# Kernel optimization log

Measured on AMD Instinct MI355X. Metric: run time of the kernel, lower is better.

The kernel has to match this reference:

```python
import jax, jax.numpy as jnp
import numpy as np
from jax import lax

# Module hyperparameters (init_kwargs)
B, T, F, H = 512, 256, 64, 128
D = F + H            # decoder LSTMCell width = input_dim + hidden_rnn
OUT_DIM = 32         # output_dim (survival horizon steps)
RISKS = 2
NEG = -1e10


def lstm_cell(x, h, c, Wih, Whh):
    # PyTorch gate order: i, f, g, o; bias=False
    g = x @ Wih.T + h @ Whh.T
    i, f, gg, o = jnp.split(g, 4, axis=-1)
    c = jax.nn.sigmoid(f) * c + jax.nn.sigmoid(i) * jnp.tanh(gg)
    h = jax.nn.sigmoid(o) * jnp.tanh(c)
    return h, c


def setup_inputs() -> dict:
    key = jax.random.key(0)
    ks = jax.random.split(key, 12)
    rn = lambda k, shp, fan: jax.random.normal(k, shp, jnp.float32) * (1.0 / np.sqrt(fan))
    return {
        "x": jax.random.normal(ks[0], (B, T, F), jnp.float32),
        # encoder LSTM (1 layer, bias=False)
        "W_ih_emb": rn(ks[1], (4 * H, F), F),
        "W_hh_emb": rn(ks[2], (4 * H, H), H),
        # longitudinal head: Linear(H -> F)
        "W_long": rn(ks[3], (F, H), H),
        "b_long": jnp.zeros((F,), jnp.float32),
        # attention head: Linear(F+H -> 1)
        "W_att": rn(ks[4], (1, D), D),
        "b_att": jnp.zeros((1,), jnp.float32),
        # per-risk cause-specific LSTMCell (bias=False) and Linear(D -> 1)
        "W_ih_cs": rn(ks[5], (RISKS, 4 * D, D), D),
        "W_hh_cs": rn(ks[6], (RISKS, 4 * D, D), D),
        "W_cs": rn(ks[7], (RISKS, 1, D), D),
        "b_cs": jnp.zeros((RISKS, 1), jnp.float32),
    }


def _forward(x, W_ih_emb, W_hh_emb, W_long, b_long, W_att, b_att,
             W_ih_cs, W_hh_cs, W_cs, b_cs):
    inputmask = jnp.abs(x).sum(2) == 0                      # [B,T]
    last_obs = (~inputmask).sum(axis=1) - 1                 # [B]

    # encoder LSTM over time
    def enc_step(carry, xt):
        h, c = carry
        h, c = lstm_cell(xt, h, c, W_ih_emb, W_hh_emb)
        return (h, c), h

    h0 = jnp.zeros((x.shape[0], H), x.dtype)
    _, hs = lax.scan(enc_step, (h0, h0), x.transpose(1, 0, 2))
    hidden = hs.transpose(1, 0, 2)                          # [B,T,H]

    long_pred = hidden @ W_long.T + b_long                  # [B,T,F]

    x_last = x[jnp.arange(x.shape[0]), last_obs]            # [B,F]
    concat = jnp.concatenate(
        [hidden, jnp.broadcast_to(x_last[:, None, :], (x.shape[0], x.shape[1], F))], -1)
    scores = (concat @ W_att.T + b_att)[..., 0]             # [B,T]

    idx = jnp.arange(x.shape[1])[None, :]
    scores = jnp.where(idx >= last_obs[:, None], NEG, scores)
    att = jax.nn.softmax(scores, axis=1)
    att = jnp.where((last_obs > 0)[:, None], att, 0.0)      # rows with last_obs==0 zeroed

    hidden_att = jnp.einsum('bt,bth->bh', att, hidden)      # [B,H]
    ha = jnp.concatenate([hidden_att, x_last], 1)           # [B,D]

    state0 = (lax.stop_gradient(ha), lax.stop_gradient(ha))  # .detach() on init state
    rs = jnp.arange(OUT_DIM * RISKS) % RISKS                # k-major, r-minor loop order

    def dec_step(carry, r):
        h, c = carry
        h, c = lstm_cell(ha, h, c, W_ih_cs[r], W_hh_cs[r])
        out = jax.nn.sigmoid(h @ W_cs[r].T + b_cs[r])       # [B,1]
        return (h, c), out

    _, outs = lax.scan(dec_step, state0, rs)                # [steps,B,1]
    outcomes = jax.nn.softmax(outs[..., 0].T, axis=-1)      # [B, OUT_DIM*RISKS]
    parts = tuple(outcomes[:, i * OUT_DIM:(i + 1) * OUT_DIM] for i in range(RISKS))
    return (long_pred,) + parts


def reference(x, W_ih_emb, W_hh_emb, W_long, b_long, W_att, b_att,
              W_ih_cs, W_hh_cs, W_cs, b_cs):
    return _forward(x, W_ih_emb, W_hh_emb, W_long, b_long, W_att, b_att,
                    W_ih_cs, W_hh_cs, W_cs, b_cs)
```

## Files before the change

### kernel.cpp

```cpp
#include <hip/hip_runtime.h>
#include <stdint.h>

#define DEV __device__ __forceinline__
typedef unsigned short u16; typedef unsigned int u32; typedef unsigned long long u64;
typedef __attribute__((ext_vector_type(8))) short s8v;
typedef __attribute__((ext_vector_type(4))) float f4v;

#define Bb 512
#define Tt 256
#define Ff 64
#define Hh 128
#define Dd 192
#define L2E  1.4426950408889634f
#define L2E2 2.8853900817779268f

DEV u16 f2bf(float f){ u32 u = __builtin_bit_cast(u32, f); u32 r = (u + 0x7fffu + ((u>>16)&1u)) >> 16; return (u16)r; }
DEV float sigm(float x){ return __builtin_amdgcn_rcpf(1.0f + __expf(-x)); }
DEV float ex2(float x){ float r; asm("v_exp_f32 %0, %1" : "=v"(r) : "v"(x)); return r; }
DEV float sig2n(float y){ return __builtin_amdgcn_rcpf(1.0f + ex2(y)); }
DEV float th2 (float y){ return 1.0f - 2.0f*__builtin_amdgcn_rcpf(1.0f + ex2(y)); }
DEV u32 cvtpk(float lo, float hi){ u32 d; asm("v_cvt_pk_bf16_f32 %0, %1, %2" : "=v"(d) : "v"(lo), "v"(hi)); return d; }
DEV float blo(u32 q){ return __builtin_bit_cast(float, q<<16); }
DEV float bhi(u32 q){ return __builtin_bit_cast(float, q & 0xffff0000u); }

DEV f4v mfma16(s8v a, s8v b, f4v c){ return __builtin_amdgcn_mfma_f32_16x16x32_bf16(a, b, c, 0, 0, 0); }
DEV void barrier_lds(){ asm volatile("s_waitcnt lgkmcnt(0)\n\ts_barrier" ::: "memory"); }

DEV void dma16(const void* g, void* l){
  __builtin_amdgcn_global_load_lds((const __attribute__((address_space(1))) void*)g,
                                   (__attribute__((address_space(3))) void*)l, 16, 0, 0);
}

DEV int hxe2(int k, int c){ return (k>>5)*512 + (((k>>3)&3)*16 + c)*8 + (k&7); }

DEV s8v pack8s(const float* p, float sc){
  const float4 a = *(const float4*)p; const float4 b = *(const float4*)(p+4);
  s8v r; r[0]=(short)f2bf(a.x*sc); r[1]=(short)f2bf(a.y*sc); r[2]=(short)f2bf(a.z*sc); r[3]=(short)f2bf(a.w*sc);
  r[4]=(short)f2bf(b.x*sc); r[5]=(short)f2bf(b.y*sc); r[6]=(short)f2bf(b.z*sc); r[7]=(short)f2bf(b.w*sc); return r;
}
DEV s8v pack8(const float* p){ return pack8s(p, 1.0f); }
DEV u32 pk2(float a, float b){ return (u32)f2bf(a) | ((u32)f2bf(b)<<16); }

__global__ __launch_bounds__(64) void prelim_k(const float* __restrict__ x,
    const float* __restrict__ Watt, const float* __restrict__ batt,
    float* __restrict__ xlast, float* __restrict__ c0, int* __restrict__ lastobs)
{
  int b = blockIdx.x, tid = threadIdx.x;
  int cnt = 0;
  for (int it = 0; it < 4; ++it){
    int t = it*64 + tid;
    const float4* p = (const float4*)(x + ((size_t)b*Tt + t)*Ff);
    float s = 0.0f;
    #pragma unroll
    for (int q = 0; q < 16; ++q){ float4 v = p[q]; s += fabsf(v.x)+fabsf(v.y)+fabsf(v.z)+fabsf(v.w); }
    u64 m = __ballot(s != 0.0f);
    cnt += __popcll(m);
  }
  int last = cnt - 1;
  int li = (last < 0) ? (Tt-1) : last;
  float xl = x[((size_t)b*Tt + li)*Ff + tid];
  xlast[b*Ff + tid] = xl;
  float p = xl * Watt[Hh + tid];
  for (int off = 32; off; off >>= 1) p += __shfl_down(p, off);
  if (tid == 0){ c0[b] = (p + batt[0]) * L2E; lastobs[b] = last; }
}

__global__ __launch_bounds__(256) void prep_wd_k(const float* __restrict__ Whhcs,
    const float* __restrict__ Wihcs, u16* __restrict__ Wd, u16* __restrict__ WdIH)
{
  int idx = blockIdx.x*256 + threadIdx.x;
  int j = idx & 7, lane = (idx>>3)&63;
  int f = idx>>9;
  int kt = f % 6; int mtr = f/6;
  int mt = mtr % 48, r = mtr/48;
  int ut = mt>>2, g = mt&3;
  int row = g*Dd + ut*16 + (lane&15);
  int k = kt*32 + (lane>>4)*8 + j;
  float sc = (g == 2) ? L2E2 : -L2E;
  size_t src = ((size_t)r*768 + row)*Dd + k;
  Wd[idx]   = f2bf(Whhcs[src] * sc);
  WdIH[idx] = f2bf(Wihcs[src] * sc);
}

__global__ __launch_bounds__(64) void xw_k(const u16* __restrict__ WdIH,
    const float* __restrict__ ha, u16* __restrict__ xwg)
{
  int lane = threadIdx.x, l15 = lane&15, l4 = lane>>4;
  int cg = blockIdx.x & 3, rm = blockIdx.x >> 2;
  s8v af[6];
  #pragma unroll
  for (int kt=0;kt<6;++kt) af[kt] = *(const s8v*)(WdIH + (size_t)(rm*6+kt)*512 + lane*8);
  #pragma unroll
  for (int ct=0; ct<8; ++ct){
    int c = cg*128 + ct*16 + l15;
    f4v a = {0,0,0,0};
    #pragma unroll
    for (int kt=0;kt<6;++kt){
      s8v b = pack8(ha + (size_t)c*Dd + kt*32 + l4*8);
      a = mfma16(af[kt], b, a);
    }
    int bg = cg*8 + ct;
    int base = bg*24576 + rm*256 + l15*16 + l4*4;
    *(u32*)&xwg[base]   = pk2(a[0], a[1]);
    *(u32*)&xwg[base+2] = pk2(a[2], a[3]);
  }
}

__global__ __launch_bounds__(512)
__attribute__((amdgpu_waves_per_eu(2,2)))
void enc_k(
    const float* __restrict__ x, const float* __restrict__ Whh, const float* __restrict__ Wih,
    const float* __restrict__ Wlong, const float* __restrict__ blong, const float* __restrict__ Watt,
    const float* __restrict__ xlast, const float* __restrict__ c0v, const int* __restrict__ lastobs,
    float* __restrict__ lp_out, float* __restrict__ ha)
{
  __shared__ __align__(16) u16 hx[2][3072];
  __shared__ float sarr[2][16];
  const int tid = threadIdx.x, wid = tid>>6, lane = tid&63, l15 = lane&15, l4 = lane>>4;
  const int b0 = blockIdx.x*16;
  const int xrow = tid>>5, xc2 = (tid&31)*2;

  s8v wf[4][6];
  #pragma unroll
  for (int mt = 0; mt < 4; ++mt){
    int gate = mt*Hh + wid*16 + l15;
    float sc = (mt == 2) ? L2E2 : -L2E;
    #pragma unroll
    for (int kt = 0; kt < 6; ++kt){
      int k0 = kt*32 + l4*8;
      if (kt < 4) wf[mt][kt] = pack8s(Whh + (size_t)gate*Hh + k0, sc);
      else        wf[mt][kt] = pack8s(Wih + (size_t)gate*Ff + (k0 - Hh), sc);
    }
  }
  s8v wfx[6];
  {
    s8v z = {0,0,0,0,0,0,0,0};
    #pragma unroll
    for (int kt = 0; kt < 6; ++kt) wfx[kt] = z;
    if (wid < 4){
      int f = wid*16 + l15;
      #pragma unroll
      for (int kt = 0; kt < 4; ++kt) wfx[kt] = pack8(Wlong + (size_t)f*Hh + kt*32 + l4*8);
    } else if (wid == 4 && l15 == 0){
      #pragma unroll
      for (int kt = 0; kt < 4; ++kt) wfx[kt] = pack8s(Watt + kt*32 + l4*8, L2E);
    }
  }
  float bl[4] = {0,0,0,0};
  if (wid < 4){
    #pragma unroll
    for (int j = 0; j < 4; ++j) bl[j] = blong[wid*16 + l4*4 + j];
  }
  const int   lastb = lastobs[b0 + l15];
  const float c0b   = c0v[b0 + l15];

  const int he0 = hxe2(wid*16 + l4*4, l15);
  const int xe0 = hxe2(Hh + xc2, xrow);
  float* lpb = lp_out + ((size_t)(b0+l15)*Tt)*Ff + wid*16 + l4*4;

  ((u64*)hx[0])[tid] = 0ull;
  {
    float2 xv = *(const float2*)(x + ((size_t)(b0+xrow)*Tt + 0)*Ff + xc2);
    *(u32*)&hx[0][xe0] = cvtpk(xv.x, xv.y);
  }
  float2 xa = *(const float2*)(x + ((size_t)(b0+xrow)*Tt + 1)*Ff + xc2);
  float2 xb;
  __syncthreads();

  float cst[4] = {0,0,0,0}, hp[4] = {0,0,0,0}, hpp[4] = {0,0,0,0};
  float accA[4] = {0,0,0,0}, mrun = -3.0e38f, zrun = 0.0f;

#define ENC_STEP(T_, CURB_, NXTB_, XC_, XN_) { \
    const int t = (T_); \
    s8v bf[6]; \
    _Pragma("unroll") \
    for (int kt = 0; kt < 6; ++kt) \
      bf[kt] = *(const s8v*)&hx[CURB_][kt*512 + lane*8]; \
    { int tp = t + 2; if (tp > Tt-1) tp = Tt-1; \
      XN_ = *(const float2*)(x + ((size_t)(b0+xrow)*Tt + tp)*Ff + xc2); } \
    f4v acc0 = {0,0,0,0}, acc1 = {0,0,0,0}, acc2 = {0,0,0,0}, acc3 = {0,0,0,0}, accx = {0,0,0,0}; \
    _Pragma("unroll") \
    for (int kt = 0; kt < 6; ++kt){ \
      acc0 = mfma16(wf[0][kt], bf[kt], acc0); \
      acc1 = mfma16(wf[1][kt], bf[kt], acc1); \
      acc2 = mfma16(wf[2][kt], bf[kt], acc2); \
      acc3 = mfma16(wf[3][kt], bf[kt], acc3); \
    } \
    if (wid < 5){ \
      _Pragma("unroll") \
      for (int kt = 0; kt < 6; ++kt) accx = mfma16(wfx[kt], bf[kt], accx); \
    } \
    if (wid == 4 && l4 == 0) sarr[NXTB_][l15] = accx[0] + c0b; \
    float hnew[4]; \
    _Pragma("unroll") \
    for (int j = 0; j < 4; ++j){ \
      float si = sig2n(acc0[j]), sf = sig2n(acc1[j]); \
      float tg = th2(acc2[j]),   so = sig2n(acc3[j]); \
      float cn = sf*cst[j] + si*tg; \
      cst[j] = cn; \
      hnew[j] = so * th2(cn * L2E2); \
    } \
    if (t >= 2){ \
      float sv = sarr[CURB_][l15]; \
      if (t-2 < lastb){ \
        float mn = fmaxf(mrun, sv); \
        float sc = ex2(mrun - mn); \
        float e  = ex2(sv - mn); \
        zrun = zrun*sc + e; \
        _Pragma("unroll") \
        for (int j = 0; j < 4; ++j) accA[j] = accA[j]*sc + e*hpp[j]; \
        mrun = mn; \
      } \
    } \
    _Pragma("unroll") \
    for (int j = 0; j < 4; ++j){ hpp[j] = hp[j]; hp[j] = hnew[j]; } \
    { u32 plo = cvtpk(hnew[0], hnew[1]), phi = cvtpk(hnew[2], hnew[3]); \
      *(u64*)&hx[NXTB_][he0] = (u64)plo | ((u64)phi<<32); } \
    if (t < Tt-1) *(u32*)&hx[NXTB_][xe0] = cvtpk(XC_.x, XC_.y); \
    if (wid < 4 && t >= 1){ \
      float4 v; v.x = accx[0]+bl[0]; v.y = accx[1]+bl[1]; v.z = accx[2]+bl[2]; v.w = accx[3]+bl[3]; \
      *(float4*)(lpb + (size_t)(t-1)*Ff) = v; \
    } \
    barrier_lds(); }

  for (int tp2 = 0; tp2 < 128; ++tp2){
    ENC_STEP(2*tp2,   0, 1, xa, xb)
    ENC_STEP(2*tp2+1, 1, 0, xb, xa)
  }
#undef ENC_STEP

  {
    if (254 < lastb){
      float sv = sarr[0][l15];
      float mn = fmaxf(mrun, sv);
      float sc = ex2(mrun - mn);
      float e  = ex2(sv - mn);
      zrun = zrun*sc + e;
      #pragma unroll
      for (int j = 0; j < 4; ++j) accA[j] = accA[j]*sc + e*hpp[j];
      mrun = mn;
    }
    s8v bfE[4];
    #pragma unroll
    for (int kt = 0; kt < 4; ++kt)
      bfE[kt] = *(const s8v*)&hx[0][kt*512 + lane*8];
    if (wid < 4){
      f4v accx = {0,0,0,0};
      #pragma unroll
      for (int kt = 0; kt < 4; ++kt) accx = mfma16(wfx[kt], bfE[kt], accx);
      float4 v; v.x = accx[0]+bl[0]; v.y = accx[1]+bl[1]; v.z = accx[2]+bl[2]; v.w = accx[3]+bl[3];
      *(float4*)(lpb + (size_t)(Tt-1)*Ff) = v;
    }
    float inv = (zrun > 0.0f) ? __builtin_amdgcn_rcpf(zrun) : 0.0f;
    #pragma unroll
    for (int j = 0; j < 4; ++j)
      ha[(size_t)(b0 + l15)*Dd + wid*16 + l4*4 + j] = accA[j]*inv;
    __syncthreads();
    for (int q = tid; q < 16*Ff; q += 512){
      int r2 = q >> 6, f = q & 63;
      ha[(size_t)(b0 + r2)*Dd + Hh + f] = xlast[(b0 + r2)*Ff + f];
    }
  }
}

__global__ __launch_bounds__(768, 3)
void dec_k(const float* __restrict__ ha, const u16* __restrict__ Wd,
    const u16* __restrict__ xwg, const float* __restrict__ Wcs,
    const float* __restrict__ bcs, float* __restrict__ outs)
{
  __shared__ __align__(16) u16 hx[2][3072];
  __shared__ __align__(16) u16 wstr[12*12*512];
  __shared__ float red[2][12][16];
  const int tid = threadIdx.x, wid = tid>>6, lane = tid&63, l15 = lane&15, l4 = lane>>4;
  const int b0 = blockIdx.x*16;

  {
    int k = (tid>>4)*4, c = tid&15;
    float4 v = *(const float4*)(ha + (size_t)(b0+c)*Dd + k);
    int e = hxe2(k, c);
    *(u32*)&hx[0][e]   = cvtpk(v.x, v.y);
    *(u32*)&hx[0][e+2] = cvtpk(v.z, v.w);
  }
  u32 xwr[2][4][2];
  #pragma unroll
  for (int r = 0; r < 2; ++r)
    #pragma unroll
    for (int g = 0; g < 4; ++g){
      int base = blockIdx.x*24576 + (r*48 + wid*4 + g)*256 + l15*16 + l4*4;
      u64 q = *(const u64*)&xwg[base];
      xwr[r][g][0] = (u32)q; xwr[r][g][1] = (u32)(q>>32);
    }
  const int u0 = wid*16 + l4*4;
  float cst[4], wcs0[4], wcs1[4];
  #pragma unroll
  for (int j = 0; j < 4; ++j){
    cst[j]  = ha[(size_t)(b0+l15)*Dd + u0 + j];
    wcs0[j] = Wcs[u0 + j];
    wcs1[j] = Wcs[Dd + u0 + j];
  }
  const float bc0 = bcs[0], bc1 = bcs[1];
  const int he0 = hxe2(u0, l15);
  u16* const wring = &wstr[wid*12*512];
  __syncthreads();

#define WSRC(R_, KT_, G_) (Wd + (size_t)(((R_)*48 + wid*4 + (G_))*6 + (KT_))*512 + lane*8)
#define ISSUE_G(RT_, KTT_, KTG_) { \
    dma16(WSRC(RT_, KTT_, 0), wring + ((4*(KTG_)+0)%12)*512); \
    dma16(WSRC(RT_, KTT_, 1), wring + ((4*(KTG_)+1)%12)*512); \
    dma16(WSRC(RT_, KTT_, 2), wring + ((4*(KTG_)+2)%12)*512); \
    dma16(WSRC(RT_, KTT_, 3), wring + ((4*(KTG_)+3)%12)*512); }
#define GRP(CURB_, KTG_) { \
    asm volatile("s_waitcnt vmcnt(8)" ::: "memory"); \
    s8v q0 = *(const s8v*)(wring + ((4*(KTG_)+0)%12)*512 + lane*8); \
    s8v q1 = *(const s8v*)(wring + ((4*(KTG_)+1)%12)*512 + lane*8); \
    s8v q2 = *(const s8v*)(wring + ((4*(KTG_)+2)%12)*512 + lane*8); \
    s8v q3 = *(const s8v*)(wring + ((4*(KTG_)+3)%12)*512 + lane*8); \
    s8v bf = *(const s8v*)&hx[CURB_][(KTG_)*512 + lane*8]; \
    a0 = mfma16(q0, bf, a0); a1 = mfma16(q1, bf, a1); \
    a2 = mfma16(q2, bf, a2); a3 = mfma16(q3, bf, a3); }

#define XWI(R_) { \
    u32 lo, hi; \
    lo = xwr[R_][0][0]; hi = xwr[R_][0][1]; a0[0]=blo(lo); a0[1]=bhi(lo); a0[2]=blo(hi); a0[3]=bhi(hi); \
    lo = xwr[R_][1][0]; hi = xwr[R_][1][1]; a1[0]=blo(lo); a1[1]=bhi(lo); a1[2]=blo(hi); a1[3]=bhi(hi); \
    lo = xwr[R_][2][0]; hi = xwr[R_][2][1]; a2[0]=blo(lo); a2[1]=bhi(lo); a2[2]=blo(hi); a2[3]=bhi(hi); \
    lo = xwr[R_][3][0]; hi = xwr[R_][3][1]; a3[0]=blo(lo); a3[1]=bhi(lo); a3[2]=blo(hi); a3[3]=bhi(hi); }

#define CELLS(WCS_, NXTB_, PAR_, BC_, S_) { \
    float part = 0.0f, hn[4]; \
    _Pragma("unroll") for (int j = 0; j < 4; ++j){ \
      float si = sig2n(a0[j]), sf = sig2n(a1[j]); \
      float tg = th2(a2[j]),   so = sig2n(a3[j]); \
      float cn = sf*cst[j] + si*tg; \
      cst[j] = cn; \
      hn[j] = so * th2(cn * L2E2); \
      part += hn[j] * WCS_[j]; } \
    { u32 plo = cvtpk(hn[0], hn[1]), phi = cvtpk(hn[2], hn[3]); \
      *(u64*)&hx[NXTB_][he0] = (u64)plo | ((u64)phi<<32); } \
    part += __shfl_xor(part, 16); part += __shfl_xor(part, 32); \
    if (l4 == 0) red[PAR_][wid][l15] = part; \
    barrier_lds(); \
    if (tid < 16){ \
      float ss = BC_; \
      _Pragma("unroll") for (int q = 0; q < 12; ++q) ss += red[PAR_][q][tid]; \
      outs[(S_)*Bb + b0 + tid] = sigm(ss); } }

#define DEC_STEP(R_, RN_, CURB_, NXTB_, WCS_, BC_, PAR_, S_) { \
    f4v a0, a1, a2, a3; \
    XWI(R_) \
    GRP(CURB_, 0) ISSUE_G(R_,  3, 0) \
    GRP(CURB_, 1) ISSUE_G(R_,  4, 1) \
    GRP(CURB_, 2) ISSUE_G(R_,  5, 2) \
    GRP(CURB_, 3) ISSUE_G(RN_, 0, 3) \
    GRP(CURB_, 4) ISSUE_G(RN_, 1, 4) \
    GRP(CURB_, 5) ISSUE_G(RN_, 2, 5) \
    CELLS(WCS_, NXTB_, PAR_, BC_, S_) }

  ISSUE_G(0, 0, 0); ISSUE_G(0, 1, 1); ISSUE_G(0, 2, 2);

  for (int sp = 0; sp < 32; ++sp){
    DEC_STEP(0, 1, 0, 1, wcs0, bc0, 0, sp*2)
    DEC_STEP(1, 0, 1, 0, wcs1, bc1, 1, sp*2+1)
  }
  asm volatile("s_waitcnt vmcnt(0)" ::: "memory");
#undef WSRC
#undef ISSUE_G
#undef GRP
#undef XWI
#undef CELLS
#undef DEC_STEP
}

__global__ __launch_bounds__(256) void fin_k(const float* __restrict__ outs, float* __restrict__ dout)
{
  int row = blockIdx.x*256 + threadIdx.x;
  float v[64]; float mx = -3.0e38f;
  #pragma unroll
  for (int s = 0; s < 64; ++s){ v[s] = outs[s*Bb + row]; mx = fmaxf(mx, v[s]); }
  float sum = 0.0f;
  #pragma unroll
  for (int s = 0; s < 64; ++s){ v[s] = __expf(v[s] - mx); sum += v[s]; }
  float inv = __builtin_amdgcn_rcpf(sum);
  float* p0 = dout + (size_t)Bb*Tt*Ff;
  float* p1 = p0 + Bb*32;
  #pragma unroll
  for (int j = 0; j < 32; ++j) p0[row*32 + j] = v[j]*inv;
  #pragma unroll
  for (int j = 0; j < 32; ++j) p1[row*32 + j] = v[32 + j]*inv;
}

extern "C" void kernel_launch(void* const* d_in, const int* in_sizes, int n_in,
                              void* d_out, int out_size, void* d_ws, size_t ws_size,
                              hipStream_t stream)
{
  const float* x      = (const float*)d_in[0];
  const float* Wih    = (const float*)d_in[1];
  const float* Whh    = (const float*)d_in[2];
  const float* Wlong  = (const float*)d_in[3];
  const float* blong  = (const float*)d_in[4];
  const float* Watt   = (const float*)d_in[5];
  const float* batt   = (const float*)d_in[6];
  const float* Wihcs  = (const float*)d_in[7];
  const float* Whhcs  = (const float*)d_in[8];
  const float* Wcs    = (const float*)d_in[9];
  const float* bcs    = (const float*)d_in[10];
  float* out = (float*)d_out;
  char* ws = (char*)d_ws;

  float* xlast   = (float*)ws;
  float* c0      = (float*)(ws + 131072);
  int*   lastobs = (int*)  (ws + 133120);
  float* ha      = (float*)(ws + 135168);
  u16*   Wd      = (u16*)  (ws + 528384);
  u16*   WdIH    = (u16*)  (ws + 1118208);
  u16*   xwg     = (u16*)  (ws + 1708032);
  float* outs    = (float*)(ws + 3280896);

  prep_wd_k<<<1152, 256, 0, stream>>>(Whhcs, Wihcs, Wd, WdIH);
  prelim_k<<<Bb, 64, 0, stream>>>(x, Watt, batt, xlast, c0, lastobs);
  enc_k<<<32, 512, 0, stream>>>(x, Whh, Wih, Wlong, blong, Watt, xlast, c0, lastobs, out, ha);
  xw_k<<<384, 64, 0, stream>>>(WdIH, ha, xwg);
  dec_k<<<32, 768, 0, stream>>>(ha, Wd, xwg, Wcs, bcs, outs);
  fin_k<<<2, 256, 0, stream>>>(outs, out);
}
```

Baseline: 546.8 us.

## Merge prep kernels, cut LSTM cell reciprocals, hoist decoder LDS loads

```diff
diff --git a/kernel.cpp b/kernel.cpp
--- a/kernel.cpp
+++ b/kernel.cpp
@@ -17,8 +17,6 @@
 DEV u16 f2bf(float f){ u32 u = __builtin_bit_cast(u32, f); u32 r = (u + 0x7fffu + ((u>>16)&1u)) >> 16; return (u16)r; }
 DEV float sigm(float x){ return __builtin_amdgcn_rcpf(1.0f + __expf(-x)); }
 DEV float ex2(float x){ float r; asm("v_exp_f32 %0, %1" : "=v"(r) : "v"(x)); return r; }
-DEV float sig2n(float y){ return __builtin_amdgcn_rcpf(1.0f + ex2(y)); }
-DEV float th2 (float y){ return 1.0f - 2.0f*__builtin_amdgcn_rcpf(1.0f + ex2(y)); }
 DEV u32 cvtpk(float lo, float hi){ u32 d; asm("v_cvt_pk_bf16_f32 %0, %1, %2" : "=v"(d) : "v"(lo), "v"(hi)); return d; }
 DEV float blo(u32 q){ return __builtin_bit_cast(float, q<<16); }
 DEV float bhi(u32 q){ return __builtin_bit_cast(float, q & 0xffff0000u); }
@@ -41,45 +39,54 @@
 DEV s8v pack8(const float* p){ return pack8s(p, 1.0f); }
 DEV u32 pk2(float a, float b){ return (u32)f2bf(a) | ((u32)f2bf(b)<<16); }
 
-__global__ __launch_bounds__(64) void prelim_k(const float* __restrict__ x,
-    const float* __restrict__ Watt, const float* __restrict__ batt,
+#define CELL7_J(A0_, A1_, A2_, A3_, CSTJ_, HNJ_) { \
+    float I_ = ex2(A0_), F_ = ex2(A1_), G_ = ex2(A2_), O_ = ex2(A3_); \
+    float Aq = (1.0f + I_)*(G_ + 1.0f), Bq = 1.0f + F_; \
+    float r1 = __builtin_amdgcn_rcpf(Aq*Bq); \
+    float cn = r1*((CSTJ_)*Aq + Bq*(G_ - 1.0f)); \
+    CSTJ_ = cn; \
+    float CN_ = ex2(cn * L2E2); \
+    float r2 = __builtin_amdgcn_rcpf((1.0f + O_)*(CN_ + 1.0f)); \
+    HNJ_ = (CN_ - 1.0f)*r2; }
+
+__global__ __launch_bounds__(256) void prep_all_k(const float* __restrict__ Whhcs,
+    const float* __restrict__ Wihcs, u16* __restrict__ Wd, u16* __restrict__ WdIH,
+    const float* __restrict__ x, const float* __restrict__ Watt, const float* __restrict__ batt,
     float* __restrict__ xlast, float* __restrict__ c0, int* __restrict__ lastobs)
 {
-  int b = blockIdx.x, tid = threadIdx.x;
-  int cnt = 0;
-  for (int it = 0; it < 4; ++it){
-    int t = it*64 + tid;
-    const float4* p = (const float4*)(x + ((size_t)b*Tt + t)*Ff);
-    float s = 0.0f;
-    #pragma unroll
-    for (int q = 0; q < 16; ++q){ float4 v = p[q]; s += fabsf(v.x)+fabsf(v.y)+fabsf(v.z)+fabsf(v.w); }
-    u64 m = __ballot(s != 0.0f);
-    cnt += __popcll(m);
-  }
-  int last = cnt - 1;
-  int li = (last < 0) ? (Tt-1) : last;
-  float xl = x[((size_t)b*Tt + li)*Ff + tid];
-  xlast[b*Ff + tid] = xl;
-  float p = xl * Watt[Hh + tid];
-  for (int off = 32; off; off >>= 1) p += __shfl_down(p, off);
-  if (tid == 0){ c0[b] = (p + batt[0]) * L2E; lastobs[b] = last; }
-}
-
-__global__ __launch_bounds__(256) void prep_wd_k(const float* __restrict__ Whhcs,
-    const float* __restrict__ Wihcs, u16* __restrict__ Wd, u16* __restrict__ WdIH)
-{
-  int idx = blockIdx.x*256 + threadIdx.x;
-  int j = idx & 7, lane = (idx>>3)&63;
-  int f = idx>>9;
-  int kt = f % 6; int mtr = f/6;
-  int mt = mtr % 48, r = mtr/48;
-  int ut = mt>>2, g = mt&3;
-  int row = g*Dd + ut*16 + (lane&15);
-  int k = kt*32 + (lane>>4)*8 + j;
-  float sc = (g == 2) ? L2E2 : -L2E;
-  size_t src = ((size_t)r*768 + row)*Dd + k;
-  Wd[idx]   = f2bf(Whhcs[src] * sc);
-  WdIH[idx] = f2bf(Wihcs[src] * sc);
+  if (blockIdx.x < 1152){
+    int idx = blockIdx.x*256 + threadIdx.x;
+    int j = idx & 7, lane = (idx>>3)&63;
+    int f = idx>>9;
+    int kt = f % 6; int mtr = f/6;
+    int mt = mtr % 48, r = mtr/48;
+    int ut = mt>>2, g = mt&3;
+    int row = g*Dd + ut*16 + (lane&15);
+    int k = kt*32 + (lane>>4)*8 + j;
+    float sc = (g == 2) ? L2E2 : -L2E;
+    size_t src = ((size_t)r*768 + row)*Dd + k;
+    Wd[idx]   = f2bf(Whhcs[src] * sc);
+    WdIH[idx] = f2bf(Wihcs[src] * sc);
+  } else if (threadIdx.x < 64){
+    int b = blockIdx.x - 1152, tid = threadIdx.x;
+    int cnt = 0;
+    for (int it = 0; it < 4; ++it){
+      int t = it*64 + tid;
+      const float4* p = (const float4*)(x + ((size_t)b*Tt + t)*Ff);
+      float s = 0.0f;
+      #pragma unroll
+      for (int q = 0; q < 16; ++q){ float4 v = p[q]; s += fabsf(v.x)+fabsf(v.y)+fabsf(v.z)+fabsf(v.w); }
+      u64 m = __ballot(s != 0.0f);
+      cnt += __popcll(m);
+    }
+    int last = cnt - 1;
+    int li = (last < 0) ? (Tt-1) : last;
+    float xl = x[((size_t)b*Tt + li)*Ff + tid];
+    xlast[b*Ff + tid] = xl;
+    float p = xl * Watt[Hh + tid];
+    for (int off = 32; off; off >>= 1) p += __shfl_down(p, off);
+    if (tid == 0){ c0[b] = (p + batt[0]) * L2E; lastobs[b] = last; }
+  }
 }
 
 __global__ __launch_bounds__(64) void xw_k(const u16* __restrict__ WdIH,
@@ -194,11 +201,7 @@
     float hnew[4]; \
     _Pragma("unroll") \
     for (int j = 0; j < 4; ++j){ \
-      float si = sig2n(acc0[j]), sf = sig2n(acc1[j]); \
-      float tg = th2(acc2[j]),   so = sig2n(acc3[j]); \
-      float cn = sf*cst[j] + si*tg; \
-      cst[j] = cn; \
-      hnew[j] = so * th2(cn * L2E2); \
+      CELL7_J(acc0[j], acc1[j], acc2[j], acc3[j], cst[j], hnew[j]) \
     } \
     if (t >= 2){ \
       float sv = sarr[CURB_][l15]; \
@@ -309,15 +312,14 @@
     dma16(WSRC(RT_, KTT_, 1), wring + ((4*(KTG_)+1)%12)*512); \
     dma16(WSRC(RT_, KTT_, 2), wring + ((4*(KTG_)+2)%12)*512); \
     dma16(WSRC(RT_, KTT_, 3), wring + ((4*(KTG_)+3)%12)*512); }
-#define GRP(CURB_, KTG_) { \
+#define GRP(KTG_) { \
     asm volatile("s_waitcnt vmcnt(8)" ::: "memory"); \
     s8v q0 = *(const s8v*)(wring + ((4*(KTG_)+0)%12)*512 + lane*8); \
     s8v q1 = *(const s8v*)(wring + ((4*(KTG_)+1)%12)*512 + lane*8); \
     s8v q2 = *(const s8v*)(wring + ((4*(KTG_)+2)%12)*512 + lane*8); \
     s8v q3 = *(const s8v*)(wring + ((4*(KTG_)+3)%12)*512 + lane*8); \
-    s8v bf = *(const s8v*)&hx[CURB_][(KTG_)*512 + lane*8]; \
-    a0 = mfma16(q0, bf, a0); a1 = mfma16(q1, bf, a1); \
-    a2 = mfma16(q2, bf, a2); a3 = mfma16(q3, bf, a3); }
+    a0 = mfma16(q0, bfs[KTG_], a0); a1 = mfma16(q1, bfs[KTG_], a1); \
+    a2 = mfma16(q2, bfs[KTG_], a2); a3 = mfma16(q3, bfs[KTG_], a3); }
 
 #define XWI(R_) { \
     u32 lo, hi; \
@@ -329,11 +331,7 @@
 #define CELLS(WCS_, NXTB_, PAR_, BC_, S_) { \
     float part = 0.0f, hn[4]; \
     _Pragma("unroll") for (int j = 0; j < 4; ++j){ \
-      float si = sig2n(a0[j]), sf = sig2n(a1[j]); \
-      float tg = th2(a2[j]),   so = sig2n(a3[j]); \
-      float cn = sf*cst[j] + si*tg; \
-      cst[j] = cn; \
-      hn[j] = so * th2(cn * L2E2); \
+      CELL7_J(a0[j], a1[j], a2[j], a3[j], cst[j], hn[j]) \
       part += hn[j] * WCS_[j]; } \
     { u32 plo = cvtpk(hn[0], hn[1]), phi = cvtpk(hn[2], hn[3]); \
       *(u64*)&hx[NXTB_][he0] = (u64)plo | ((u64)phi<<32); } \
@@ -346,14 +344,17 @@
       outs[(S_)*Bb + b0 + tid] = sigm(ss); } }
 
 #define DEC_STEP(R_, RN_, CURB_, NXTB_, WCS_, BC_, PAR_, S_) { \
+    s8v bfs[6]; \
+    _Pragma("unroll") \
+    for (int kt = 0; kt < 6; ++kt) bfs[kt] = *(const s8v*)&hx[CURB_][kt*512 + lane*8]; \
     f4v a0, a1, a2, a3; \
     XWI(R_) \
-    GRP(CURB_, 0) ISSUE_G(R_,  3, 0) \
-    GRP(CURB_, 1) ISSUE_G(R_,  4, 1) \
-    GRP(CURB_, 2) ISSUE_G(R_,  5, 2) \
-    GRP(CURB_, 3) ISSUE_G(RN_, 0, 3) \
-    GRP(CURB_, 4) ISSUE_G(RN_, 1, 4) \
-    GRP(CURB_, 5) ISSUE_G(RN_, 2, 5) \
+    GRP(0) ISSUE_G(R_,  3, 0) \
+    GRP(1) ISSUE_G(R_,  4, 1) \
+    GRP(2) ISSUE_G(R_,  5, 2) \
+    GRP(3) ISSUE_G(RN_, 0, 3) \
+    GRP(4) ISSUE_G(RN_, 1, 4) \
+    GRP(5) ISSUE_G(RN_, 2, 5) \
     CELLS(WCS_, NXTB_, PAR_, BC_, S_) }
 
   ISSUE_G(0, 0, 0); ISSUE_G(0, 1, 1); ISSUE_G(0, 2, 2);
@@ -416,8 +417,7 @@
   u16*   xwg     = (u16*)  (ws + 1708032);
   float* outs    = (float*)(ws + 3280896);
 
-  prep_wd_k<<<1152, 256, 0, stream>>>(Whhcs, Wihcs, Wd, WdIH);
-  prelim_k<<<Bb, 64, 0, stream>>>(x, Watt, batt, xlast, c0, lastobs);
+  prep_all_k<<<1664, 256, 0, stream>>>(Whhcs, Wihcs, Wd, WdIH, x, Watt, batt, xlast, c0, lastobs);
   enc_k<<<32, 512, 0, stream>>>(x, Whh, Wih, Wlong, blong, Watt, xlast, c0, lastobs, out, ha);
   xw_k<<<384, 64, 0, stream>>>(WdIH, ha, xwg);
   dec_k<<<32, 768, 0, stream>>>(ha, Wd, xwg, Wcs, bcs, outs);
```

After: 569.7 us. 1.04x slower.
